# Kernel tuning notes

Measured on AMD Instinct MI355X. Metric: run time of the kernel, lower is better.

The kernel has to match this reference:

```python
import jax, jax.numpy as jnp
import numpy as np


def setup_inputs() -> dict:
    key = jax.random.key(0)
    ks = jax.random.split(key, 7)
    B, T, DIN, D = 64, 512, 512, 512
    s_in = 1.0 / np.sqrt(DIN)  # ~glorot-ish scale for input kernels
    s_h = 1.0 / np.sqrt(D)     # scale for recurrent kernels (orthogonal-ish magnitude)
    return {
        "X": jax.random.normal(ks[0], (B, T, DIN), jnp.float32),
        "W_z": jax.random.normal(ks[1], (DIN, D), jnp.float32) * s_in,
        "U_z": jax.random.normal(ks[2], (D, D), jnp.float32) * s_h,
        "b_z": jnp.zeros((D,), jnp.float32),
        "W_r": jax.random.normal(ks[3], (DIN, D), jnp.float32) * s_in,
        "U_r": jax.random.normal(ks[4], (D, D), jnp.float32) * s_h,
        "b_r": jnp.zeros((D,), jnp.float32),
        "W_h": jax.random.normal(ks[5], (DIN, D), jnp.float32) * s_in,
        "U_h": jax.random.normal(ks[6], (D, D), jnp.float32) * s_h,
        "b_h": jnp.zeros((D,), jnp.float32),
        "mask": jnp.ones((B, T), jnp.int32),
    }


def reference(X, W_z, U_z, b_z, W_r, U_r, b_r, W_h, U_h, b_h, mask):
    # X: [B, T, DIN] -> time-major [T, B, DIN]
    Xt = jnp.transpose(X, (1, 0, 2))
    # Precompute input projections (large GEMMs, done once): [T, B, D]
    xz = Xt @ W_z + b_z
    xr = Xt @ W_r + b_r
    xh = Xt @ W_h + b_h
    # Padded/shifted mask (pad=1): step t sees mask[t-1]; step 0 sees 0,
    # which zeroes the (zero) initial state exactly as in the theano code.
    m = jnp.transpose(mask, (1, 0)).astype(X.dtype)[:, :, None]  # [T, B, 1]
    m_tm1 = jnp.concatenate([jnp.zeros_like(m[:1]), m[:-1]], axis=0)

    B = X.shape[0]
    D = W_z.shape[1]
    h0 = jnp.zeros((B, D), X.dtype)

    def step(h_tm1, inputs):
        xz_t, xr_t, xh_t, mt = inputs
        hm = mt * h_tm1                                  # masked previous state
        z = jax.nn.sigmoid(xz_t + hm @ U_z)              # update gate
        r = jax.nn.sigmoid(xr_t + hm @ U_r)              # reset gate
        hh = jnp.tanh(xh_t + (r * hm) @ U_h)             # candidate
        h_t = z * hm + (1.0 - z) * hh
        return h_t, None

    h_last, _ = jax.lax.scan(step, h0, (xz, xr, xh, m_tm1))
    # return_sequences=False -> last hidden state [B, D]
    return h_last
```

## Files before the change

### kernel.cpp

```cpp
#include <hip/hip_runtime.h>
#include <hip/hip_fp16.h>

#define B_   64
#define T_   512
#define DINc 512
#define D_   512
#define NWG  16
#define JS   32

typedef _Float16 half8 __attribute__((ext_vector_type(8)));
typedef _Float16 half4 __attribute__((ext_vector_type(4)));
typedef float   floatx4 __attribute__((ext_vector_type(4)));
typedef unsigned uintx4 __attribute__((ext_vector_type(4)));

#define WAITV(N) asm volatile("s_waitcnt vmcnt(" #N ")" ::: "memory")
#define SCB()    __builtin_amdgcn_sched_barrier(0)

__global__ __launch_bounds__(256) void k_cvtX(const float* __restrict__ X, _Float16* __restrict__ Xh) {
    int idx = blockIdx.x * 256 + threadIdx.x;
    int m  = idx >> 6;
    int k8 = idx & 63;
    int b = m & 63, t = m >> 6;
    const float* src = X + ((size_t)(b * T_ + t)) * DINc + k8 * 8;
    float4 f0 = *(const float4*)(src);
    float4 f1 = *(const float4*)(src + 4);
    half8 h;
    h[0] = (_Float16)f0.x; h[1] = (_Float16)f0.y; h[2] = (_Float16)f0.z; h[3] = (_Float16)f0.w;
    h[4] = (_Float16)f1.x; h[5] = (_Float16)f1.y; h[6] = (_Float16)f1.z; h[7] = (_Float16)f1.w;
    *(half8*)(Xh + (size_t)m * DINc + k8 * 8) = h;
}

__global__ __launch_bounds__(256) void k_cvtW(const float* __restrict__ M0, const float* __restrict__ M1,
                                              const float* __restrict__ M2, _Float16* __restrict__ Mt) {
    __shared__ float tile[64][65];
    int g = blockIdx.z;
    const float* W = (g == 0) ? M0 : ((g == 1) ? M1 : M2);
    int n0 = blockIdx.x * 64, k0 = blockIdx.y * 64;
    int c = threadIdx.x & 63, r4 = threadIdx.x >> 6;
#pragma unroll
    for (int i = 0; i < 16; ++i) {
        int k = r4 + i * 4;
        tile[k][c] = W[(size_t)(k0 + k) * D_ + n0 + c];
    }
    __syncthreads();
    _Float16* out = Mt + (size_t)g * D_ * DINc;
#pragma unroll
    for (int i = 0; i < 16; ++i) {
        int n = r4 + i * 4;
        out[(size_t)(n0 + n) * DINc + k0 + c] = (_Float16)tile[c][n];
    }
}

__global__ __launch_bounds__(256) void k_cvtM(const int* __restrict__ mask, float* __restrict__ maskT) {
    int idx = blockIdx.x * 256 + threadIdx.x;
    int t = idx >> 6, b = idx & 63;
    maskT[idx] = (float)mask[(size_t)b * T_ + t];
}

__global__ __launch_bounds__(256) void k_gemm(const _Float16* __restrict__ Xh, const _Float16* __restrict__ Wt,
                                              const float* __restrict__ bz, const float* __restrict__ br,
                                              const float* __restrict__ bh, _Float16* __restrict__ xprojT) {
    __shared__ _Float16 As[128 * 32];
    __shared__ _Float16 Bs[128 * 32];
    int g = blockIdx.z;
    const _Float16* Wg = Wt + (size_t)g * 512 * 512;
    const float* bias = (g == 0) ? bz : ((g == 1) ? br : bh);
    _Float16* out = xprojT + (size_t)g * 16777216;
    int mb = blockIdx.x * 128, nb = blockIdx.y * 128;
    int tid = threadIdx.x, l = tid & 63, w = tid >> 6;
    int wr = w >> 1, wc = w & 1;
    int lr = l & 15, lg = l >> 4;

    floatx4 acc[4][4] = {};

    int ga0 = tid, ga1 = tid + 256;
    int ra0 = ga0 >> 2, ca0 = (ga0 & 3) * 8;
    int ra1 = ga1 >> 2, ca1 = (ga1 & 3) * 8;

    uint4 pa0, pa1, pb0, pb1;
    pa0 = *(const uint4*)(Xh + (size_t)(mb + ra0) * 512 + ca0);
    pa1 = *(const uint4*)(Xh + (size_t)(mb + ra1) * 512 + ca1);
    pb0 = *(const uint4*)(Wg + (size_t)(nb + ra0) * 512 + ca0);
    pb1 = *(const uint4*)(Wg + (size_t)(nb + ra1) * 512 + ca1);

    for (int kt = 0; kt < 16; ++kt) {
        __syncthreads();
        *(uint4*)(&As[ga0 * 8]) = pa0;
        *(uint4*)(&As[ga1 * 8]) = pa1;
        *(uint4*)(&Bs[ga0 * 8]) = pb0;
        *(uint4*)(&Bs[ga1 * 8]) = pb1;
        __syncthreads();
        if (kt < 15) {
            int kb = (kt + 1) * 32;
            pa0 = *(const uint4*)(Xh + (size_t)(mb + ra0) * 512 + kb + ca0);
            pa1 = *(const uint4*)(Xh + (size_t)(mb + ra1) * 512 + kb + ca1);
            pb0 = *(const uint4*)(Wg + (size_t)(nb + ra0) * 512 + kb + ca0);
            pb1 = *(const uint4*)(Wg + (size_t)(nb + ra1) * 512 + kb + ca1);
        }
        half8 af[4], bf[4];
#pragma unroll
        for (int mi = 0; mi < 4; mi++) af[mi] = *(const half8*)(&As[(wr * 64 + mi * 16 + lr) * 32 + lg * 8]);
#pragma unroll
        for (int ni = 0; ni < 4; ni++) bf[ni] = *(const half8*)(&Bs[(wc * 64 + ni * 16 + lr) * 32 + lg * 8]);
#pragma unroll
        for (int mi = 0; mi < 4; mi++)
#pragma unroll
            for (int ni = 0; ni < 4; ni++)
                acc[mi][ni] = __builtin_amdgcn_mfma_f32_16x16x32_f16(af[mi], bf[ni], acc[mi][ni], 0, 0, 0);
    }

#pragma unroll
    for (int ni = 0; ni < 4; ni++) {
        int col = nb + wc * 64 + ni * 16 + lr;
        float bv = bias[col];
#pragma unroll
        for (int mi = 0; mi < 4; mi++) {
            int row = mb + wr * 64 + mi * 16 + lg * 4;
            int tt = row >> 6, bb = row & 63;
            half4 hv;
#pragma unroll
            for (int i = 0; i < 4; i++) hv[i] = (_Float16)(acc[mi][ni][i] + bv);
            *(half4*)(out + (size_t)tt * 32768 + (size_t)col * 64 + bb) = hv;
        }
    }
}

__device__ __forceinline__ void st_agent(unsigned long long* p, unsigned long long v) {
    __hip_atomic_store(p, v, __ATOMIC_RELAXED, __HIP_MEMORY_SCOPE_AGENT);
}
__device__ __forceinline__ unsigned ld_flag(const unsigned* p) {
    return __hip_atomic_load(p, __ATOMIC_RELAXED, __HIP_MEMORY_SCOPE_AGENT);
}
__device__ __forceinline__ void st_flag(unsigned* p, unsigned v) {
    __hip_atomic_store(p, v, __ATOMIC_RELAXED, __HIP_MEMORY_SCOPE_AGENT);
}
__device__ __forceinline__ uintx4 ld16_agent(const void* p) {
    uintx4 r;
    asm volatile("global_load_dwordx4 %0, %1, off sc0 sc1" : "=v"(r) : "v"(p) : "memory");
    return r;
}

__device__ __forceinline__ unsigned long long pack_quad(const float v4[4], int lr) {
    unsigned long long unit = 0;
    int j = lr & 3;
#pragma unroll
    for (int i = 0; i < 4; i++) {
        _Float16 hv = (_Float16)v4[i];
        unsigned int v = (unsigned int)__builtin_bit_cast(unsigned short, hv);
        unsigned int o1 = __shfl_xor(v, 1, 64);
        unsigned int pair = (lr & 1) ? (o1 | (v << 16)) : (v | (o1 << 16));
        unsigned int q2 = __shfl_xor(pair, 2, 64);
        unsigned long long u = (lr & 2) ? ((unsigned long long)q2 | ((unsigned long long)pair << 32))
                                        : ((unsigned long long)pair | ((unsigned long long)q2 << 32));
        if (i == j) unit = u;
    }
    return unit;
}

__device__ __forceinline__ void poll_flags(const unsigned* f, unsigned need, int l) {
    for (;;) {
        unsigned v0 = ld_flag(f + l * 16);
        unsigned v1 = ld_flag(f + (64 + l) * 16);
        if (__all(v0 >= need && v1 >= need)) break;
    }
    SCB();
}

__global__ __launch_bounds__(512) void k_scan(const _Float16* __restrict__ Ut,
                                              const float* __restrict__ maskT,
                                              const _Float16* __restrict__ xprojT,
                                              unsigned long long* __restrict__ hbuf,
                                              unsigned long long* __restrict__ rhbuf,
                                              unsigned* __restrict__ fh, unsigned* __restrict__ fr,
                                              float* __restrict__ out) {
    __shared__ __align__(16) _Float16 Ulds[2 * JS * 512];
    __shared__ __align__(16) _Float16 Stg[64 * 512];
    char* StgB = (char*)Stg;
    int tid = threadIdx.x, l = tid & 63, w = tid >> 6;
    int lr = l & 15, lg = l >> 4;
    int mt = w >> 1, nt = w & 1;
    int slot = blockIdx.x;
    int jsb = slot * JS;
    const int fidx = slot * 8 + w;

    for (int c = tid; c < 2 * JS * 64; c += 512) {
        int g  = c >> 11;
        int n  = (c >> 6) & 31;
        int k16 = c & 63;
        uintx4 v = *(const uintx4*)(Ut + (size_t)g * 262144 + (size_t)(jsb + n) * 512 + k16 * 8);
        *(uintx4*)((char*)Ulds + g * 32768 + n * 1024 + ((k16 * 16) ^ ((n & 7) << 4))) = v;
    }
    half8 uhf[16];
    {
        const _Float16* UtH = Ut + (size_t)2 * 262144;
        int ncol = jsb + nt * 16 + lr;
#pragma unroll
        for (int j = 0; j < 16; j++)
            uhf[j] = *(const half8*)(UtH + (size_t)ncol * 512 + j * 32 + lg * 8);
    }
    __syncthreads();

    const char* UB = (const char*)Ulds + (nt * 16 + lr) * 1024;
    const int swz = (lr & 7) << 4;

    int row0 = mt * 16 + lg * 4;
    int colg = jsb + nt * 16 + lr;

    float h4[4]  = {0.f, 0.f, 0.f, 0.f};
    float hm4[4] = {0.f, 0.f, 0.f, 0.f};

    const int punit = (mt * 16 + lg * 4 + (lr & 3)) * 128 + ((jsb + nt * 16) >> 2) + ((lr >> 2) & 3);
    const char* SB = StgB + (mt * 16 + lr) * 1024;

    const _Float16* xzB = xprojT + (size_t)colg * 64 + row0;
    const _Float16* xrB = xzB + (size_t)16777216;
    const _Float16* xhB = xrB + (size_t)16777216;

    {
        half4 xz0 = *(const half4*)(xzB);
        half4 xh0 = *(const half4*)(xhB);
        float4 m0 = *(const float4*)(maskT + row0);
#pragma unroll
        for (int i = 0; i < 4; i++) {
            float z  = __builtin_amdgcn_rcpf(1.f + __expf(-(float)xz0[i]));
            float hh = tanhf((float)xh0[i]);
            h4[i]  = (1.f - z) * hh;
            hm4[i] = ((float)m0[i]) * h4[i];
        }
        st_agent(hbuf + punit, pack_quad(hm4, lr));
        WAITV(0);
        if (l == 0) st_flag(fh + fidx * 16, 1u);
    }

    for (int t = 1; t < T_; ++t) {
        const char* hmG = (const char*)(hbuf + ((t - 1) & 1) * 8192);
        unsigned long long* rhW = rhbuf + (t & 1) * 8192;
        unsigned long long* hW  = hbuf  + (t & 1) * 8192;
        const char* rhG = (const char*)rhW;

        half4 xzp = *(const half4*)(xzB + (size_t)t * 32768);
        half4 xrp = *(const half4*)(xrB + (size_t)t * 32768);
        half4 xhp = *(const half4*)(xhB + (size_t)t * 32768);
        float4 mv = *(const float4*)(maskT + (size_t)t * 64 + row0);

        __syncthreads();
        poll_flags(fh, (unsigned)t, l);
        {
            uintx4 gg[8];
#pragma unroll
            for (int it = 0; it < 8; ++it)
                gg[it] = ld16_agent(hmG + (w * 8 + it) * 1024 + l * 16);
            WAITV(4); SCB();
#pragma unroll
            for (int it = 0; it < 4; ++it)
                *(uintx4*)(StgB + (w * 8 + it) * 1024 + ((l * 16) ^ (it << 4))) = gg[it];
            WAITV(0); SCB();
#pragma unroll
            for (int it = 4; it < 8; ++it)
                *(uintx4*)(StgB + (w * 8 + it) * 1024 + ((l * 16) ^ (it << 4))) = gg[it];
        }
        __syncthreads();
        half8 af[16];
#pragma unroll
        for (int j = 0; j < 16; j++)
            af[j] = *(const half8*)(SB + ((j * 64 + lg * 16) ^ swz));
        floatx4 accr = {0.f, 0.f, 0.f, 0.f};
#pragma unroll
        for (int j = 0; j < 16; j++) {
            int boff = (j * 64 + lg * 16) ^ swz;
            half8 br8 = *(const half8*)(UB + 32768 + boff);
            accr = __builtin_amdgcn_mfma_f32_16x16x32_f16(af[j], br8, accr, 0, 0, 0);
        }
        float rh4[4];
#pragma unroll
        for (int i = 0; i < 4; i++) {
            float rr = __builtin_amdgcn_rcpf(1.f + __expf(-((float)xrp[i] + accr[i])));
            rh4[i] = rr * hm4[i];
        }
        st_agent(rhW + punit, pack_quad(rh4, lr));
        WAITV(0);
        if (l == 0) st_flag(fr + fidx * 16, (unsigned)t);
        floatx4 accz = {0.f, 0.f, 0.f, 0.f};
#pragma unroll
        for (int j = 0; j < 16; j++) {
            int boff = (j * 64 + lg * 16) ^ swz;
            half8 bz8 = *(const half8*)(UB + boff);
            accz = __builtin_amdgcn_mfma_f32_16x16x32_f16(af[j], bz8, accz, 0, 0, 0);
        }
        float z4[4];
#pragma unroll
        for (int i = 0; i < 4; i++)
            z4[i] = __builtin_amdgcn_rcpf(1.f + __expf(-((float)xzp[i] + accz[i])));

        __syncthreads();
        poll_flags(fr, (unsigned)t, l);
        {
            uintx4 gg[8];
#pragma unroll
            for (int it = 0; it < 8; ++it)
                gg[it] = ld16_agent(rhG + (w * 8 + it) * 1024 + l * 16);
            WAITV(4); SCB();
#pragma unroll
            for (int it = 0; it < 4; ++it)
                *(uintx4*)(StgB + (w * 8 + it) * 1024 + ((l * 16) ^ (it << 4))) = gg[it];
            WAITV(0); SCB();
#pragma unroll
            for (int it = 4; it < 8; ++it)
                *(uintx4*)(StgB + (w * 8 + it) * 1024 + ((l * 16) ^ (it << 4))) = gg[it];
        }
        __syncthreads();
        half8 af2[16];
#pragma unroll
        for (int j = 0; j < 16; j++)
            af2[j] = *(const half8*)(SB + ((j * 64 + lg * 16) ^ swz));
        floatx4 acch0 = {0.f, 0.f, 0.f, 0.f}, acch1 = {0.f, 0.f, 0.f, 0.f};
#pragma unroll
        for (int j = 0; j < 16; j += 2) {
            acch0 = __builtin_amdgcn_mfma_f32_16x16x32_f16(af2[j],     uhf[j],     acch0, 0, 0, 0);
            acch1 = __builtin_amdgcn_mfma_f32_16x16x32_f16(af2[j + 1], uhf[j + 1], acch1, 0, 0, 0);
        }
#pragma unroll
        for (int i = 0; i < 4; i++) {
            float hh = tanhf((float)xhp[i] + acch0[i] + acch1[i]);
            h4[i]  = z4[i] * hm4[i] + (1.f - z4[i]) * hh;
            hm4[i] = ((float)mv[i]) * h4[i];
        }
        st_agent(hW + punit, pack_quad(hm4, lr));
        WAITV(0);
        if (l == 0) st_flag(fh + fidx * 16, (unsigned)(t + 1));
    }

#pragma unroll
    for (int i = 0; i < 4; i++)
        out[(size_t)(row0 + i) * 512 + colg] = h4[i];
}

extern "C" void kernel_launch(void* const* d_in, const int* in_sizes, int n_in,
                              void* d_out, int out_size, void* d_ws, size_t ws_size,
                              hipStream_t stream) {
    (void)in_sizes; (void)n_in; (void)out_size; (void)ws_size;
    const float* X  = (const float*)d_in[0];
    const float* Wz = (const float*)d_in[1];
    const float* Uz = (const float*)d_in[2];
    const float* bz = (const float*)d_in[3];
    const float* Wr = (const float*)d_in[4];
    const float* Ur = (const float*)d_in[5];
    const float* br = (const float*)d_in[6];
    const float* Wh = (const float*)d_in[7];
    const float* Uh = (const float*)d_in[8];
    const float* bh = (const float*)d_in[9];
    const int* mask = (const int*)d_in[10];
    float* out = (float*)d_out;

    char* ws = (char*)d_ws;
    unsigned* fh = (unsigned*)ws;
    unsigned* fr = (unsigned*)(ws + 8192);
    unsigned long long* hbuf  = (unsigned long long*)(ws + 16384);
    unsigned long long* rhbuf = (unsigned long long*)(ws + 16384 + 131072);
    _Float16* Xh     = (_Float16*)(ws + 16384 + 2 * 131072);
    _Float16* Wt     = (_Float16*)(ws + 16384 + 2 * 131072 + 33554432);
    _Float16* Ut     = (_Float16*)(ws + 16384 + 2 * 131072 + 33554432 + 1572864);
    _Float16* xprojT = (_Float16*)(ws + 16384 + 2 * 131072 + 33554432 + 2 * 1572864);
    float*    maskT  = (float*)(ws + 16384 + 2 * 131072 + 33554432 + 2 * 1572864 + 100663296);

    hipMemsetAsync(ws, 0, 16384, stream);
    hipLaunchKernelGGL(k_cvtX, dim3(8192), dim3(256), 0, stream, X, Xh);
    hipLaunchKernelGGL(k_cvtW, dim3(8, 8, 3), dim3(256), 0, stream, Wz, Wr, Wh, Wt);
    hipLaunchKernelGGL(k_cvtW, dim3(8, 8, 3), dim3(256), 0, stream, Uz, Ur, Uh, Ut);
    hipLaunchKernelGGL(k_cvtM, dim3(128), dim3(256), 0, stream, mask, maskT);
    hipLaunchKernelGGL(k_gemm, dim3(256, 4, 3), dim3(256), 0, stream, Xh, Wt, bz, br, bh, xprojT);
    hipLaunchKernelGGL(k_scan, dim3(NWG), dim3(512), 0, stream, Ut, maskT, xprojT,
                       hbuf, rhbuf, fh, fr, out);
}
```

Measured before the change: 3.764 ms.

## Halve scan workgroups to 8, each covering 64 hidden columns with 2 row tiles

The persistent recurrent scan now runs on 8 workgroups of 64 hidden columns each instead of 16 of 32. Each wave covers one 16-column tile across two 16-row batch tiles. U_r and U_h live in registers and only U_z stays in LDS. Fewer participants should make the per-step cross-workgroup flag polling cheaper (one flag load per lane instead of two). In exchange, each workgroup does twice the MFMA work per step on the serial critical path and carries more register pressure.

```diff
diff --git a/kernel.cpp b/kernel.cpp
--- a/kernel.cpp
+++ b/kernel.cpp
@@ -5,8 +5,8 @@
 #define T_   512
 #define DINc 512
 #define D_   512
-#define NWG  16
-#define JS   32
+#define NWG  8
+#define JS   64
 
 typedef _Float16 half8 __attribute__((ext_vector_type(8)));
 typedef _Float16 half4 __attribute__((ext_vector_type(4)));
@@ -159,9 +159,8 @@
 
 __device__ __forceinline__ void poll_flags(const unsigned* f, unsigned need, int l) {
     for (;;) {
-        unsigned v0 = ld_flag(f + l * 16);
-        unsigned v1 = ld_flag(f + (64 + l) * 16);
-        if (__all(v0 >= need && v1 >= need)) break;
+        unsigned v = ld_flag(f + l * 16);
+        if (__all(v >= need)) break;
     }
     SCB();
 }
@@ -173,61 +172,71 @@
                                               unsigned long long* __restrict__ rhbuf,
                                               unsigned* __restrict__ fh, unsigned* __restrict__ fr,
                                               float* __restrict__ out) {
-    __shared__ __align__(16) _Float16 Ulds[2 * JS * 512];
+    __shared__ __align__(16) _Float16 Ulds[JS * 512];
     __shared__ __align__(16) _Float16 Stg[64 * 512];
     char* StgB = (char*)Stg;
     int tid = threadIdx.x, l = tid & 63, w = tid >> 6;
     int lr = l & 15, lg = l >> 4;
-    int mt = w >> 1, nt = w & 1;
+    int nt  = w >> 1;
+    int mt2 = w & 1;
+    int m0 = mt2 * 16, m1 = m0 + 32;
     int slot = blockIdx.x;
     int jsb = slot * JS;
     const int fidx = slot * 8 + w;
 
-    for (int c = tid; c < 2 * JS * 64; c += 512) {
-        int g  = c >> 11;
-        int n  = (c >> 6) & 31;
+    for (int c = tid; c < JS * 64; c += 512) {
+        int n   = c >> 6;
         int k16 = c & 63;
-        uintx4 v = *(const uintx4*)(Ut + (size_t)g * 262144 + (size_t)(jsb + n) * 512 + k16 * 8);
-        *(uintx4*)((char*)Ulds + g * 32768 + n * 1024 + ((k16 * 16) ^ ((n & 7) << 4))) = v;
-    }
-    half8 uhf[16];
+        uintx4 v = *(const uintx4*)(Ut + (size_t)(jsb + n) * 512 + k16 * 8);
+        *(uintx4*)((char*)Ulds + n * 1024 + ((k16 * 16) ^ ((n & 7) << 4))) = v;
+    }
+    half8 urf[16], uhf[16];
     {
+        const _Float16* UtR = Ut + (size_t)262144;
         const _Float16* UtH = Ut + (size_t)2 * 262144;
         int ncol = jsb + nt * 16 + lr;
 #pragma unroll
-        for (int j = 0; j < 16; j++)
+        for (int j = 0; j < 16; j++) {
+            urf[j] = *(const half8*)(UtR + (size_t)ncol * 512 + j * 32 + lg * 8);
             uhf[j] = *(const half8*)(UtH + (size_t)ncol * 512 + j * 32 + lg * 8);
+        }
     }
     __syncthreads();
 
     const char* UB = (const char*)Ulds + (nt * 16 + lr) * 1024;
     const int swz = (lr & 7) << 4;
 
-    int row0 = mt * 16 + lg * 4;
     int colg = jsb + nt * 16 + lr;
-
-    float h4[4]  = {0.f, 0.f, 0.f, 0.f};
-    float hm4[4] = {0.f, 0.f, 0.f, 0.f};
-
-    const int punit = (mt * 16 + lg * 4 + (lr & 3)) * 128 + ((jsb + nt * 16) >> 2) + ((lr >> 2) & 3);
-    const char* SB = StgB + (mt * 16 + lr) * 1024;
-
-    const _Float16* xzB = xprojT + (size_t)colg * 64 + row0;
+    int row0 = m0 + lg * 4;
+    int row1 = m1 + lg * 4;
+
+    float h4[2][4]  = {};
+    float hm4[2][4] = {};
+
+    const int punit0 = (m0 + lg * 4 + (lr & 3)) * 128 + ((jsb + nt * 16) >> 2) + ((lr >> 2) & 3);
+    const int punit1 = (m1 + lg * 4 + (lr & 3)) * 128 + ((jsb + nt * 16) >> 2) + ((lr >> 2) & 3);
+    const char* SB0 = StgB + (m0 + lr) * 1024;
+    const char* SB1 = StgB + (m1 + lr) * 1024;
+
+    const _Float16* xzB = xprojT + (size_t)colg * 64;
     const _Float16* xrB = xzB + (size_t)16777216;
     const _Float16* xhB = xrB + (size_t)16777216;
 
     {
-        half4 xz0 = *(const half4*)(xzB);
-        half4 xh0 = *(const half4*)(xhB);
-        float4 m0 = *(const float4*)(maskT + row0);
+        half4 xz0a = *(const half4*)(xzB + row0), xz0b = *(const half4*)(xzB + row1);
+        half4 xh0a = *(const half4*)(xhB + row0), xh0b = *(const half4*)(xhB + row1);
+        float4 m0a = *(const float4*)(maskT + row0), m0b = *(const float4*)(maskT + row1);
 #pragma unroll
         for (int i = 0; i < 4; i++) {
-            float z  = __builtin_amdgcn_rcpf(1.f + __expf(-(float)xz0[i]));
-            float hh = tanhf((float)xh0[i]);
-            h4[i]  = (1.f - z) * hh;
-            hm4[i] = ((float)m0[i]) * h4[i];
-        }
-        st_agent(hbuf + punit, pack_quad(hm4, lr));
+            float za = __builtin_amdgcn_rcpf(1.f + __expf(-(float)xz0a[i]));
+            float zb = __builtin_amdgcn_rcpf(1.f + __expf(-(float)xz0b[i]));
+            h4[0][i] = (1.f - za) * tanhf((float)xh0a[i]);
+            h4[1][i] = (1.f - zb) * tanhf((float)xh0b[i]);
+            hm4[0][i] = ((float)m0a[i]) * h4[0][i];
+            hm4[1][i] = ((float)m0b[i]) * h4[1][i];
+        }
+        st_agent(hbuf + punit0, pack_quad(hm4[0], lr));
+        st_agent(hbuf + punit1, pack_quad(hm4[1], lr));
         WAITV(0);
         if (l == 0) st_flag(fh + fidx * 16, 1u);
     }
@@ -238,10 +247,14 @@
         unsigned long long* hW  = hbuf  + (t & 1) * 8192;
         const char* rhG = (const char*)rhW;
 
-        half4 xzp = *(const half4*)(xzB + (size_t)t * 32768);
-        half4 xrp = *(const half4*)(xrB + (size_t)t * 32768);
-        half4 xhp = *(const half4*)(xhB + (size_t)t * 32768);
-        float4 mv = *(const float4*)(maskT + (size_t)t * 64 + row0);
+        const _Float16* xzT = xzB + (size_t)t * 32768;
+        const _Float16* xrT = xrB + (size_t)t * 32768;
+        const _Float16* xhT = xhB + (size_t)t * 32768;
+        half4 xzp0 = *(const half4*)(xzT + row0), xzp1 = *(const half4*)(xzT + row1);
+        half4 xrp0 = *(const half4*)(xrT + row0), xrp1 = *(const half4*)(xrT + row1);
+        half4 xhp0 = *(const half4*)(xhT + row0), xhp1 = *(const half4*)(xhT + row1);
+        float4 mva = *(const float4*)(maskT + (size_t)t * 64 + row0);
+        float4 mvb = *(const float4*)(maskT + (size_t)t * 64 + row1);
 
         __syncthreads();
         poll_flags(fh, (unsigned)t, l);
@@ -260,37 +273,43 @@
                 *(uintx4*)(StgB + (w * 8 + it) * 1024 + ((l * 16) ^ (it << 4))) = gg[it];
         }
         __syncthreads();
-        half8 af[16];
-#pragma unroll
-        for (int j = 0; j < 16; j++)
-            af[j] = *(const half8*)(SB + ((j * 64 + lg * 16) ^ swz));
-        floatx4 accr = {0.f, 0.f, 0.f, 0.f};
+        floatx4 accr0 = {}, accr1 = {};
+#pragma unroll
+        for (int j = 0; j < 16; j++) {
+            int aoff = (j * 64 + lg * 16) ^ swz;
+            half8 a0 = *(const half8*)(SB0 + aoff);
+            half8 a1 = *(const half8*)(SB1 + aoff);
+            accr0 = __builtin_amdgcn_mfma_f32_16x16x32_f16(a0, urf[j], accr0, 0, 0, 0);
+            accr1 = __builtin_amdgcn_mfma_f32_16x16x32_f16(a1, urf[j], accr1, 0, 0, 0);
+        }
+        float rh4[2][4];
+#pragma unroll
+        for (int i = 0; i < 4; i++) {
+            float r0 = __builtin_amdgcn_rcpf(1.f + __expf(-((float)xrp0[i] + accr0[i])));
+            float r1 = __builtin_amdgcn_rcpf(1.f + __expf(-((float)xrp1[i] + accr1[i])));
+            rh4[0][i] = r0 * hm4[0][i];
+            rh4[1][i] = r1 * hm4[1][i];
+        }
+        st_agent(rhW + punit0, pack_quad(rh4[0], lr));
+        st_agent(rhW + punit1, pack_quad(rh4[1], lr));
+        WAITV(0);
+        if (l == 0) st_flag(fr + fidx * 16, (unsigned)t);
+        floatx4 accz0 = {}, accz1 = {};
 #pragma unroll
         for (int j = 0; j < 16; j++) {
             int boff = (j * 64 + lg * 16) ^ swz;
-            half8 br8 = *(const half8*)(UB + 32768 + boff);
-            accr = __builtin_amdgcn_mfma_f32_16x16x32_f16(af[j], br8, accr, 0, 0, 0);
-        }
-        float rh4[4];
+            half8 a0 = *(const half8*)(SB0 + boff);
+            half8 a1 = *(const half8*)(SB1 + boff);
+            half8 bz = *(const half8*)(UB + boff);
+            accz0 = __builtin_amdgcn_mfma_f32_16x16x32_f16(a0, bz, accz0, 0, 0, 0);
+            accz1 = __builtin_amdgcn_mfma_f32_16x16x32_f16(a1, bz, accz1, 0, 0, 0);
+        }
+        float z4[2][4];
 #pragma unroll
         for (int i = 0; i < 4; i++) {
-            float rr = __builtin_amdgcn_rcpf(1.f + __expf(-((float)xrp[i] + accr[i])));
-            rh4[i] = rr * hm4[i];
-        }
-        st_agent(rhW + punit, pack_quad(rh4, lr));
-        WAITV(0);
-        if (l == 0) st_flag(fr + fidx * 16, (unsigned)t);
-        floatx4 accz = {0.f, 0.f, 0.f, 0.f};
-#pragma unroll
-        for (int j = 0; j < 16; j++) {
-            int boff = (j * 64 + lg * 16) ^ swz;
-            half8 bz8 = *(const half8*)(UB + boff);
-            accz = __builtin_amdgcn_mfma_f32_16x16x32_f16(af[j], bz8, accz, 0, 0, 0);
-        }
-        float z4[4];
-#pragma unroll
-        for (int i = 0; i < 4; i++)
-            z4[i] = __builtin_amdgcn_rcpf(1.f + __expf(-((float)xzp[i] + accz[i])));
+            z4[0][i] = __builtin_amdgcn_rcpf(1.f + __expf(-((float)xzp0[i] + accz0[i])));
+            z4[1][i] = __builtin_amdgcn_rcpf(1.f + __expf(-((float)xzp1[i] + accz1[i])));
+        }
 
         __syncthreads();
         poll_flags(fr, (unsigned)t, l);
@@ -309,30 +328,35 @@
                 *(uintx4*)(StgB + (w * 8 + it) * 1024 + ((l * 16) ^ (it << 4))) = gg[it];
         }
         __syncthreads();
-        half8 af2[16];
-#pragma unroll
-        for (int j = 0; j < 16; j++)
-            af2[j] = *(const half8*)(SB + ((j * 64 + lg * 16) ^ swz));
-        floatx4 acch0 = {0.f, 0.f, 0.f, 0.f}, acch1 = {0.f, 0.f, 0.f, 0.f};
-#pragma unroll
-        for (int j = 0; j < 16; j += 2) {
-            acch0 = __builtin_amdgcn_mfma_f32_16x16x32_f16(af2[j],     uhf[j],     acch0, 0, 0, 0);
-            acch1 = __builtin_amdgcn_mfma_f32_16x16x32_f16(af2[j + 1], uhf[j + 1], acch1, 0, 0, 0);
+        floatx4 acch0 = {}, acch1 = {};
+#pragma unroll
+        for (int j = 0; j < 16; j++) {
+            int aoff = (j * 64 + lg * 16) ^ swz;
+            half8 a0 = *(const half8*)(SB0 + aoff);
+            half8 a1 = *(const half8*)(SB1 + aoff);
+            acch0 = __builtin_amdgcn_mfma_f32_16x16x32_f16(a0, uhf[j], acch0, 0, 0, 0);
+            acch1 = __builtin_amdgcn_mfma_f32_16x16x32_f16(a1, uhf[j], acch1, 0, 0, 0);
         }
 #pragma unroll
         for (int i = 0; i < 4; i++) {
-            float hh = tanhf((float)xhp[i] + acch0[i] + acch1[i]);
-            h4[i]  = z4[i] * hm4[i] + (1.f - z4[i]) * hh;
-            hm4[i] = ((float)mv[i]) * h4[i];
-        }
-        st_agent(hW + punit, pack_quad(hm4, lr));
+            float hha = tanhf((float)xhp0[i] + acch0[i]);
+            float hhb = tanhf((float)xhp1[i] + acch1[i]);
+            h4[0][i] = z4[0][i] * hm4[0][i] + (1.f - z4[0][i]) * hha;
+            h4[1][i] = z4[1][i] * hm4[1][i] + (1.f - z4[1][i]) * hhb;
+            hm4[0][i] = ((float)mva[i]) * h4[0][i];
+            hm4[1][i] = ((float)mvb[i]) * h4[1][i];
+        }
+        st_agent(hW + punit0, pack_quad(hm4[0], lr));
+        st_agent(hW + punit1, pack_quad(hm4[1], lr));
         WAITV(0);
         if (l == 0) st_flag(fh + fidx * 16, (unsigned)(t + 1));
     }
 
 #pragma unroll
-    for (int i = 0; i < 4; i++)
-        out[(size_t)(row0 + i) * 512 + colg] = h4[i];
+    for (int i = 0; i < 4; i++) {
+        out[(size_t)(row0 + i) * 512 + colg] = h4[0][i];
+        out[(size_t)(row1 + i) * 512 + colg] = h4[1][i];
+    }
 }
 
 extern "C" void kernel_launch(void* const* d_in, const int* in_sizes, int n_in,
```

Result: slower. 6.244 ms (+65.9%).

## Compute full reset gate redundantly per workgroup to drop second grid barrier

Applied to the files above, without the earlier changes.

Each workgroup now computes the entire 64x512 reset-gate product r = sigmoid(xr + hm@U_r) locally, streaming U_r from global memory, and forms r*hm in shared memory. This removes the second cross-workgroup exchange (rhbuf store, fr flag and poll) each timestep, halving grid-wide synchronization on the serial critical path. In exchange every workgroup does 16x redundant MFMA work and reads all of U_r (512 KB) from L2 each step, plus many extra xr loads. The final timestep also skips its unnecessary state publish.

```diff
diff --git a/kernel.cpp b/kernel.cpp
--- a/kernel.cpp
+++ b/kernel.cpp
@@ -170,55 +170,61 @@
                                               const float* __restrict__ maskT,
                                               const _Float16* __restrict__ xprojT,
                                               unsigned long long* __restrict__ hbuf,
-                                              unsigned long long* __restrict__ rhbuf,
-                                              unsigned* __restrict__ fh, unsigned* __restrict__ fr,
+                                              unsigned* __restrict__ fh,
                                               float* __restrict__ out) {
-    __shared__ __align__(16) _Float16 Ulds[2 * JS * 512];
+    __shared__ __align__(16) _Float16 UzL[JS * 512];
     __shared__ __align__(16) _Float16 Stg[64 * 512];
     char* StgB = (char*)Stg;
     int tid = threadIdx.x, l = tid & 63, w = tid >> 6;
     int lr = l & 15, lg = l >> 4;
-    int mt = w >> 1, nt = w & 1;
+    int mz = w >> 1, nz = w & 1;
     int slot = blockIdx.x;
     int jsb = slot * JS;
     const int fidx = slot * 8 + w;
 
-    for (int c = tid; c < 2 * JS * 64; c += 512) {
-        int g  = c >> 11;
-        int n  = (c >> 6) & 31;
+    for (int c = tid; c < JS * 64; c += 512) {
+        int n   = c >> 6;
         int k16 = c & 63;
-        uintx4 v = *(const uintx4*)(Ut + (size_t)g * 262144 + (size_t)(jsb + n) * 512 + k16 * 8);
-        *(uintx4*)((char*)Ulds + g * 32768 + n * 1024 + ((k16 * 16) ^ ((n & 7) << 4))) = v;
+        uintx4 v = *(const uintx4*)(Ut + (size_t)(jsb + n) * 512 + k16 * 8);
+        *(uintx4*)((char*)UzL + n * 1024 + ((k16 * 16) ^ ((n & 7) << 4))) = v;
     }
     half8 uhf[16];
     {
         const _Float16* UtH = Ut + (size_t)2 * 262144;
-        int ncol = jsb + nt * 16 + lr;
+        int ncol = jsb + nz * 16 + lr;
 #pragma unroll
         for (int j = 0; j < 16; j++)
             uhf[j] = *(const half8*)(UtH + (size_t)ncol * 512 + j * 32 + lg * 8);
     }
     __syncthreads();
 
-    const char* UB = (const char*)Ulds + (nt * 16 + lr) * 1024;
     const int swz = (lr & 7) << 4;
-
-    int row0 = mt * 16 + lg * 4;
-    int colg = jsb + nt * 16 + lr;
+    const char* SA0 = StgB + (0  + lr) * 1024;
+    const char* SA1 = StgB + (16 + lr) * 1024;
+    const char* SA2 = StgB + (32 + lr) * 1024;
+    const char* SA3 = StgB + (48 + lr) * 1024;
+    const char* SAz = StgB + (mz * 16 + lr) * 1024;
+    const char* UBz = (const char*)UzL + (nz * 16 + lr) * 1024;
+    const _Float16* urB0 = Ut + 262144 + (size_t)(w * 64 +  0 + lr) * 512 + lg * 8;
+    const _Float16* urB1 = Ut + 262144 + (size_t)(w * 64 + 16 + lr) * 512 + lg * 8;
+    const _Float16* urB2 = Ut + 262144 + (size_t)(w * 64 + 32 + lr) * 512 + lg * 8;
+    const _Float16* urB3 = Ut + 262144 + (size_t)(w * 64 + 48 + lr) * 512 + lg * 8;
+
+    int row0 = mz * 16 + lg * 4;
+    int colg = jsb + nz * 16 + lr;
 
     float h4[4]  = {0.f, 0.f, 0.f, 0.f};
     float hm4[4] = {0.f, 0.f, 0.f, 0.f};
 
-    const int punit = (mt * 16 + lg * 4 + (lr & 3)) * 128 + ((jsb + nt * 16) >> 2) + ((lr >> 2) & 3);
-    const char* SB = StgB + (mt * 16 + lr) * 1024;
-
-    const _Float16* xzB = xprojT + (size_t)colg * 64 + row0;
-    const _Float16* xrB = xzB + (size_t)16777216;
-    const _Float16* xhB = xrB + (size_t)16777216;
+    const int punit = (mz * 16 + lg * 4 + (lr & 3)) * 128 + ((jsb + nz * 16) >> 2) + ((lr >> 2) & 3);
+
+    const _Float16* xzB = xprojT + (size_t)colg * 64;
+    const _Float16* xhB = xzB + (size_t)2 * 16777216;
+    const _Float16* xrG = xprojT + (size_t)16777216;
 
     {
-        half4 xz0 = *(const half4*)(xzB);
-        half4 xh0 = *(const half4*)(xhB);
+        half4 xz0 = *(const half4*)(xzB + row0);
+        half4 xh0 = *(const half4*)(xhB + row0);
         float4 m0 = *(const float4*)(maskT + row0);
 #pragma unroll
         for (int i = 0; i < 4; i++) {
@@ -234,13 +240,10 @@
 
     for (int t = 1; t < T_; ++t) {
         const char* hmG = (const char*)(hbuf + ((t - 1) & 1) * 8192);
-        unsigned long long* rhW = rhbuf + (t & 1) * 8192;
-        unsigned long long* hW  = hbuf  + (t & 1) * 8192;
-        const char* rhG = (const char*)rhW;
-
-        half4 xzp = *(const half4*)(xzB + (size_t)t * 32768);
-        half4 xrp = *(const half4*)(xrB + (size_t)t * 32768);
-        half4 xhp = *(const half4*)(xhB + (size_t)t * 32768);
+        unsigned long long* hW = hbuf + (t & 1) * 8192;
+
+        half4 xzp = *(const half4*)(xzB + (size_t)t * 32768 + row0);
+        half4 xhp = *(const half4*)(xhB + (size_t)t * 32768 + row0);
         float4 mv = *(const float4*)(maskT + (size_t)t * 64 + row0);
 
         __syncthreads();
@@ -260,74 +263,98 @@
                 *(uintx4*)(StgB + (w * 8 + it) * 1024 + ((l * 16) ^ (it << 4))) = gg[it];
         }
         __syncthreads();
-        half8 af[16];
-#pragma unroll
-        for (int j = 0; j < 16; j++)
-            af[j] = *(const half8*)(SB + ((j * 64 + lg * 16) ^ swz));
-        floatx4 accr = {0.f, 0.f, 0.f, 0.f};
+
+        floatx4 racc[4][4] = {};
+        floatx4 zacc = {};
+        half8 bb0 = *(const half8*)(urB0);
+        half8 bb1 = *(const half8*)(urB1);
+        half8 bb2 = *(const half8*)(urB2);
+        half8 bb3 = *(const half8*)(urB3);
 #pragma unroll
         for (int j = 0; j < 16; j++) {
-            int boff = (j * 64 + lg * 16) ^ swz;
-            half8 br8 = *(const half8*)(UB + 32768 + boff);
-            accr = __builtin_amdgcn_mfma_f32_16x16x32_f16(af[j], br8, accr, 0, 0, 0);
-        }
-        float rh4[4];
+            int aoff = (j * 64 + lg * 16) ^ swz;
+            half8 a0 = *(const half8*)(SA0 + aoff);
+            half8 a1 = *(const half8*)(SA1 + aoff);
+            half8 a2 = *(const half8*)(SA2 + aoff);
+            half8 a3 = *(const half8*)(SA3 + aoff);
+            half8 az = *(const half8*)(SAz + aoff);
+            half8 bz = *(const half8*)(UBz + aoff);
+            half8 nb0, nb1, nb2, nb3;
+            if (j < 15) {
+                nb0 = *(const half8*)(urB0 + (j + 1) * 32);
+                nb1 = *(const half8*)(urB1 + (j + 1) * 32);
+                nb2 = *(const half8*)(urB2 + (j + 1) * 32);
+                nb3 = *(const half8*)(urB3 + (j + 1) * 32);
+            }
+            zacc = __builtin_amdgcn_mfma_f32_16x16x32_f16(az, bz, zacc, 0, 0, 0);
+            racc[0][0] = __builtin_amdgcn_mfma_f32_16x16x32_f16(a0, bb0, racc[0][0], 0, 0, 0);
+            racc[1][0] = __builtin_amdgcn_mfma_f32_16x16x32_f16(a1, bb0, racc[1][0], 0, 0, 0);
+            racc[2][0] = __builtin_amdgcn_mfma_f32_16x16x32_f16(a2, bb0, racc[2][0], 0, 0, 0);
+            racc[3][0] = __builtin_amdgcn_mfma_f32_16x16x32_f16(a3, bb0, racc[3][0], 0, 0, 0);
+            racc[0][1] = __builtin_amdgcn_mfma_f32_16x16x32_f16(a0, bb1, racc[0][1], 0, 0, 0);
+            racc[1][1] = __builtin_amdgcn_mfma_f32_16x16x32_f16(a1, bb1, racc[1][1], 0, 0, 0);
+            racc[2][1] = __builtin_amdgcn_mfma_f32_16x16x32_f16(a2, bb1, racc[2][1], 0, 0, 0);
+            racc[3][1] = __builtin_amdgcn_mfma_f32_16x16x32_f16(a3, bb1, racc[3][1], 0, 0, 0);
+            racc[0][2] = __builtin_amdgcn_mfma_f32_16x16x32_f16(a0, bb2, racc[0][2], 0, 0, 0);
+            racc[1][2] = __builtin_amdgcn_mfma_f32_16x16x32_f16(a1, bb2, racc[1][2], 0, 0, 0);
+            racc[2][2] = __builtin_amdgcn_mfma_f32_16x16x32_f16(a2, bb2, racc[2][2], 0, 0, 0);
+            racc[3][2] = __builtin_amdgcn_mfma_f32_16x16x32_f16(a3, bb2, racc[3][2], 0, 0, 0);
+            racc[0][3] = __builtin_amdgcn_mfma_f32_16x16x32_f16(a0, bb3, racc[0][3], 0, 0, 0);
+            racc[1][3] = __builtin_amdgcn_mfma_f32_16x16x32_f16(a1, bb3, racc[1][3], 0, 0, 0);
+            racc[2][3] = __builtin_amdgcn_mfma_f32_16x16x32_f16(a2, bb3, racc[2][3], 0, 0, 0);
+            racc[3][3] = __builtin_amdgcn_mfma_f32_16x16x32_f16(a3, bb3, racc[3][3], 0, 0, 0);
+            if (j < 15) { bb0 = nb0; bb1 = nb1; bb2 = nb2; bb3 = nb3; }
+        }
+        float z4[4];
+#pragma unroll
+        for (int i = 0; i < 4; i++)
+            z4[i] = __builtin_amdgcn_rcpf(1.f + __expf(-((float)xzp[i] + zacc[i])));
+
+#pragma unroll
+        for (int m = 0; m < 4; m++)
+#pragma unroll
+            for (int nn = 0; nn < 4; nn++) {
+                half4 xr = *(const half4*)(xrG + (size_t)t * 32768 +
+                                           (size_t)(w * 64 + nn * 16 + lr) * 64 + m * 16 + lg * 4);
+#pragma unroll
+                for (int i = 0; i < 4; i++)
+                    racc[m][nn][i] = __builtin_amdgcn_rcpf(1.f + __expf(-((float)xr[i] + racc[m][nn][i])));
+            }
+        __syncthreads();
+
+#pragma unroll
+        for (int m = 0; m < 4; m++)
+#pragma unroll
+            for (int nn = 0; nn < 4; nn++) {
+                float tmp[4] = {racc[m][nn][0], racc[m][nn][1], racc[m][nn][2], racc[m][nn][3]};
+                unsigned long long u = pack_quad(tmp, lr);
+                int R  = m * 16 + lg * 4 + (lr & 3);
+                int c0 = w * 64 + nn * 16 + ((lr >> 2) & 3) * 4;
+                int byteoff = R * 1024 + (((c0 >> 3) * 16) ^ ((R & 7) << 4)) + ((c0 & 4) ? 8 : 0);
+                half4 hmu = *(half4*)(StgB + byteoff);
+                half4 ru  = __builtin_bit_cast(half4, u);
+                half4 prod = ru * hmu;
+                *(half4*)(StgB + byteoff) = prod;
+            }
+        __syncthreads();
+
+        floatx4 acch = {};
+#pragma unroll
+        for (int j = 0; j < 16; j++) {
+            half8 ah = *(const half8*)(SAz + ((j * 64 + lg * 16) ^ swz));
+            acch = __builtin_amdgcn_mfma_f32_16x16x32_f16(ah, uhf[j], acch, 0, 0, 0);
+        }
 #pragma unroll
         for (int i = 0; i < 4; i++) {
-            float rr = __builtin_amdgcn_rcpf(1.f + __expf(-((float)xrp[i] + accr[i])));
-            rh4[i] = rr * hm4[i];
-        }
-        st_agent(rhW + punit, pack_quad(rh4, lr));
-        WAITV(0);
-        if (l == 0) st_flag(fr + fidx * 16, (unsigned)t);
-        floatx4 accz = {0.f, 0.f, 0.f, 0.f};
-#pragma unroll
-        for (int j = 0; j < 16; j++) {
-            int boff = (j * 64 + lg * 16) ^ swz;
-            half8 bz8 = *(const half8*)(UB + boff);
-            accz = __builtin_amdgcn_mfma_f32_16x16x32_f16(af[j], bz8, accz, 0, 0, 0);
-        }
-        float z4[4];
-#pragma unroll
-        for (int i = 0; i < 4; i++)
-            z4[i] = __builtin_amdgcn_rcpf(1.f + __expf(-((float)xzp[i] + accz[i])));
-
-        __syncthreads();
-        poll_flags(fr, (unsigned)t, l);
-        {
-            uintx4 gg[8];
-#pragma unroll
-            for (int it = 0; it < 8; ++it)
-                gg[it] = ld16_agent(rhG + (w * 8 + it) * 1024 + l * 16);
-            WAITV(4); SCB();
-#pragma unroll
-            for (int it = 0; it < 4; ++it)
-                *(uintx4*)(StgB + (w * 8 + it) * 1024 + ((l * 16) ^ (it << 4))) = gg[it];
-            WAITV(0); SCB();
-#pragma unroll
-            for (int it = 4; it < 8; ++it)
-                *(uintx4*)(StgB + (w * 8 + it) * 1024 + ((l * 16) ^ (it << 4))) = gg[it];
-        }
-        __syncthreads();
-        half8 af2[16];
-#pragma unroll
-        for (int j = 0; j < 16; j++)
-            af2[j] = *(const half8*)(SB + ((j * 64 + lg * 16) ^ swz));
-        floatx4 acch0 = {0.f, 0.f, 0.f, 0.f}, acch1 = {0.f, 0.f, 0.f, 0.f};
-#pragma unroll
-        for (int j = 0; j < 16; j += 2) {
-            acch0 = __builtin_amdgcn_mfma_f32_16x16x32_f16(af2[j],     uhf[j],     acch0, 0, 0, 0);
-            acch1 = __builtin_amdgcn_mfma_f32_16x16x32_f16(af2[j + 1], uhf[j + 1], acch1, 0, 0, 0);
-        }
-#pragma unroll
-        for (int i = 0; i < 4; i++) {
-            float hh = tanhf((float)xhp[i] + acch0[i] + acch1[i]);
+            float hh = tanhf((float)xhp[i] + acch[i]);
             h4[i]  = z4[i] * hm4[i] + (1.f - z4[i]) * hh;
             hm4[i] = ((float)mv[i]) * h4[i];
         }
-        st_agent(hW + punit, pack_quad(hm4, lr));
-        WAITV(0);
-        if (l == 0) st_flag(fh + fidx * 16, (unsigned)(t + 1));
+        if (t < T_ - 1) {
+            st_agent(hW + punit, pack_quad(hm4, lr));
+            WAITV(0);
+            if (l == 0) st_flag(fh + fidx * 16, (unsigned)(t + 1));
+        }
     }
 
 #pragma unroll
@@ -354,9 +381,7 @@
 
     char* ws = (char*)d_ws;
     unsigned* fh = (unsigned*)ws;
-    unsigned* fr = (unsigned*)(ws + 8192);
     unsigned long long* hbuf  = (unsigned long long*)(ws + 16384);
-    unsigned long long* rhbuf = (unsigned long long*)(ws + 16384 + 131072);
     _Float16* Xh     = (_Float16*)(ws + 16384 + 2 * 131072);
     _Float16* Wt     = (_Float16*)(ws + 16384 + 2 * 131072 + 33554432);
     _Float16* Ut     = (_Float16*)(ws + 16384 + 2 * 131072 + 33554432 + 1572864);
@@ -370,5 +395,5 @@
     hipLaunchKernelGGL(k_cvtM, dim3(128), dim3(256), 0, stream, mask, maskT);
     hipLaunchKernelGGL(k_gemm, dim3(256, 4, 3), dim3(256), 0, stream, Xh, Wt, bz, br, bh, xprojT);
     hipLaunchKernelGGL(k_scan, dim3(NWG), dim3(512), 0, stream, Ut, maskT, xprojT,
-                       hbuf, rhbuf, fh, fr, out);
-}
+                       hbuf, fh, out);
+}
```

New measurement: 14.57 ms. +287.1%, slower.

## Replace flag-based cross-workgroup sync with poisoned-data polling in GRU scan

Applied to the files above, without the earlier changes.

Removes the per-wave flag stores and flag polling between workgroups. Consumers now poll the exchanged h and r*h buffers directly until no 16-byte chunk holds the all-ones poison pattern, and each workgroup re-poisons the previous parity buffer after reading it. The aim is to cut one round trip and the waitcnt serialization from every cross-CU handoff in the latency-bound recurrence, and it also raises wave priority around the MFMA loops. The risk is correctness: a valid fp16 pair could be mistaken for poison, and the relaxed re-poison stores could race with peers that have not yet read the buffer.

```diff
diff --git a/kernel.cpp b/kernel.cpp
--- a/kernel.cpp
+++ b/kernel.cpp
@@ -128,16 +128,13 @@
 __device__ __forceinline__ void st_agent(unsigned long long* p, unsigned long long v) {
     __hip_atomic_store(p, v, __ATOMIC_RELAXED, __HIP_MEMORY_SCOPE_AGENT);
 }
-__device__ __forceinline__ unsigned ld_flag(const unsigned* p) {
-    return __hip_atomic_load(p, __ATOMIC_RELAXED, __HIP_MEMORY_SCOPE_AGENT);
-}
-__device__ __forceinline__ void st_flag(unsigned* p, unsigned v) {
-    __hip_atomic_store(p, v, __ATOMIC_RELAXED, __HIP_MEMORY_SCOPE_AGENT);
-}
 __device__ __forceinline__ uintx4 ld16_agent(const void* p) {
     uintx4 r;
     asm volatile("global_load_dwordx4 %0, %1, off sc0 sc1" : "=v"(r) : "v"(p) : "memory");
     return r;
+}
+__device__ __forceinline__ bool chunk_valid(uintx4 v) {
+    return ((v[0] & v[1]) != 0xFFFFFFFFu) && ((v[2] & v[3]) != 0xFFFFFFFFu);
 }
 
 __device__ __forceinline__ unsigned long long pack_quad(const float v4[4], int lr) {
@@ -157,21 +154,11 @@
     return unit;
 }
 
-__device__ __forceinline__ void poll_flags(const unsigned* f, unsigned need, int l) {
-    for (;;) {
-        unsigned v0 = ld_flag(f + l * 16);
-        unsigned v1 = ld_flag(f + (64 + l) * 16);
-        if (__all(v0 >= need && v1 >= need)) break;
-    }
-    SCB();
-}
-
 __global__ __launch_bounds__(512) void k_scan(const _Float16* __restrict__ Ut,
                                               const float* __restrict__ maskT,
                                               const _Float16* __restrict__ xprojT,
                                               unsigned long long* __restrict__ hbuf,
                                               unsigned long long* __restrict__ rhbuf,
-                                              unsigned* __restrict__ fh, unsigned* __restrict__ fr,
                                               float* __restrict__ out) {
     __shared__ __align__(16) _Float16 Ulds[2 * JS * 512];
     __shared__ __align__(16) _Float16 Stg[64 * 512];
@@ -181,7 +168,6 @@
     int mt = w >> 1, nt = w & 1;
     int slot = blockIdx.x;
     int jsb = slot * JS;
-    const int fidx = slot * 8 + w;
 
     for (int c = tid; c < 2 * JS * 64; c += 512) {
         int g  = c >> 11;
@@ -228,14 +214,14 @@
             hm4[i] = ((float)m0[i]) * h4[i];
         }
         st_agent(hbuf + punit, pack_quad(hm4, lr));
-        WAITV(0);
-        if (l == 0) st_flag(fh + fidx * 16, 1u);
     }
 
     for (int t = 1; t < T_; ++t) {
         const char* hmG = (const char*)(hbuf + ((t - 1) & 1) * 8192);
-        unsigned long long* rhW = rhbuf + (t & 1) * 8192;
-        unsigned long long* hW  = hbuf  + (t & 1) * 8192;
+        unsigned long long* rhPsn = rhbuf + ((t - 1) & 1) * 8192;
+        unsigned long long* hPsn  = hbuf  + ((t - 1) & 1) * 8192;
+        unsigned long long* rhW   = rhbuf + (t & 1) * 8192;
+        unsigned long long* hW    = hbuf  + (t & 1) * 8192;
         const char* rhG = (const char*)rhW;
 
         half4 xzp = *(const half4*)(xzB + (size_t)t * 32768);
@@ -243,34 +229,44 @@
         half4 xhp = *(const half4*)(xhB + (size_t)t * 32768);
         float4 mv = *(const float4*)(maskT + (size_t)t * 64 + row0);
 
-        __syncthreads();
-        poll_flags(fh, (unsigned)t, l);
+        uintx4 gg[8];
         {
-            uintx4 gg[8];
+            unsigned vmask = 0;
 #pragma unroll
             for (int it = 0; it < 8; ++it)
                 gg[it] = ld16_agent(hmG + (w * 8 + it) * 1024 + l * 16);
-            WAITV(4); SCB();
-#pragma unroll
-            for (int it = 0; it < 4; ++it)
-                *(uintx4*)(StgB + (w * 8 + it) * 1024 + ((l * 16) ^ (it << 4))) = gg[it];
             WAITV(0); SCB();
 #pragma unroll
-            for (int it = 4; it < 8; ++it)
-                *(uintx4*)(StgB + (w * 8 + it) * 1024 + ((l * 16) ^ (it << 4))) = gg[it];
-        }
+            for (int it = 0; it < 8; ++it) if (chunk_valid(gg[it])) vmask |= 1u << it;
+            while (!__all(vmask == 255u)) {
+#pragma unroll
+                for (int it = 0; it < 8; ++it)
+                    if (!(vmask & (1u << it)))
+                        gg[it] = ld16_agent(hmG + (w * 8 + it) * 1024 + l * 16);
+                WAITV(0); SCB();
+#pragma unroll
+                for (int it = 0; it < 8; ++it) if (chunk_valid(gg[it])) vmask |= 1u << it;
+            }
+        }
+        st_agent(rhPsn + punit, ~0ull);
+        __syncthreads();
+#pragma unroll
+        for (int it = 0; it < 8; ++it)
+            *(uintx4*)(StgB + (w * 8 + it) * 1024 + ((l * 16) ^ (it << 4))) = gg[it];
         __syncthreads();
         half8 af[16];
 #pragma unroll
         for (int j = 0; j < 16; j++)
             af[j] = *(const half8*)(SB + ((j * 64 + lg * 16) ^ swz));
         floatx4 accr = {0.f, 0.f, 0.f, 0.f};
+        __builtin_amdgcn_s_setprio(1);
 #pragma unroll
         for (int j = 0; j < 16; j++) {
             int boff = (j * 64 + lg * 16) ^ swz;
             half8 br8 = *(const half8*)(UB + 32768 + boff);
             accr = __builtin_amdgcn_mfma_f32_16x16x32_f16(af[j], br8, accr, 0, 0, 0);
         }
+        __builtin_amdgcn_s_setprio(0);
         float rh4[4];
 #pragma unroll
         for (int i = 0; i < 4; i++) {
@@ -278,56 +274,65 @@
             rh4[i] = rr * hm4[i];
         }
         st_agent(rhW + punit, pack_quad(rh4, lr));
-        WAITV(0);
-        if (l == 0) st_flag(fr + fidx * 16, (unsigned)t);
         floatx4 accz = {0.f, 0.f, 0.f, 0.f};
+        __builtin_amdgcn_s_setprio(1);
 #pragma unroll
         for (int j = 0; j < 16; j++) {
             int boff = (j * 64 + lg * 16) ^ swz;
             half8 bz8 = *(const half8*)(UB + boff);
             accz = __builtin_amdgcn_mfma_f32_16x16x32_f16(af[j], bz8, accz, 0, 0, 0);
         }
+        __builtin_amdgcn_s_setprio(0);
         float z4[4];
 #pragma unroll
         for (int i = 0; i < 4; i++)
             z4[i] = __builtin_amdgcn_rcpf(1.f + __expf(-((float)xzp[i] + accz[i])));
 
-        __syncthreads();
-        poll_flags(fr, (unsigned)t, l);
+        uintx4 gg2[8];
         {
-            uintx4 gg[8];
+            unsigned vmask = 0;
 #pragma unroll
             for (int it = 0; it < 8; ++it)
-                gg[it] = ld16_agent(rhG + (w * 8 + it) * 1024 + l * 16);
-            WAITV(4); SCB();
-#pragma unroll
-            for (int it = 0; it < 4; ++it)
-                *(uintx4*)(StgB + (w * 8 + it) * 1024 + ((l * 16) ^ (it << 4))) = gg[it];
+                gg2[it] = ld16_agent(rhG + (w * 8 + it) * 1024 + l * 16);
             WAITV(0); SCB();
 #pragma unroll
-            for (int it = 4; it < 8; ++it)
-                *(uintx4*)(StgB + (w * 8 + it) * 1024 + ((l * 16) ^ (it << 4))) = gg[it];
-        }
+            for (int it = 0; it < 8; ++it) if (chunk_valid(gg2[it])) vmask |= 1u << it;
+            while (!__all(vmask == 255u)) {
+#pragma unroll
+                for (int it = 0; it < 8; ++it)
+                    if (!(vmask & (1u << it)))
+                        gg2[it] = ld16_agent(rhG + (w * 8 + it) * 1024 + l * 16);
+                WAITV(0); SCB();
+#pragma unroll
+                for (int it = 0; it < 8; ++it) if (chunk_valid(gg2[it])) vmask |= 1u << it;
+            }
+        }
+        st_agent(hPsn + punit, ~0ull);
+        __syncthreads();
+#pragma unroll
+        for (int it = 0; it < 8; ++it)
+            *(uintx4*)(StgB + (w * 8 + it) * 1024 + ((l * 16) ^ (it << 4))) = gg2[it];
         __syncthreads();
         half8 af2[16];
 #pragma unroll
         for (int j = 0; j < 16; j++)
             af2[j] = *(const half8*)(SB + ((j * 64 + lg * 16) ^ swz));
         floatx4 acch0 = {0.f, 0.f, 0.f, 0.f}, acch1 = {0.f, 0.f, 0.f, 0.f};
+        __builtin_amdgcn_s_setprio(1);
 #pragma unroll
         for (int j = 0; j < 16; j += 2) {
             acch0 = __builtin_amdgcn_mfma_f32_16x16x32_f16(af2[j],     uhf[j],     acch0, 0, 0, 0);
             acch1 = __builtin_amdgcn_mfma_f32_16x16x32_f16(af2[j + 1], uhf[j + 1], acch1, 0, 0, 0);
         }
+        __builtin_amdgcn_s_setprio(0);
 #pragma unroll
         for (int i = 0; i < 4; i++) {
             float hh = tanhf((float)xhp[i] + acch0[i] + acch1[i]);
             h4[i]  = z4[i] * hm4[i] + (1.f - z4[i]) * hh;
             hm4[i] = ((float)mv[i]) * h4[i];
         }
-        st_agent(hW + punit, pack_quad(hm4, lr));
-        WAITV(0);
-        if (l == 0) st_flag(fh + fidx * 16, (unsigned)(t + 1));
+        if (t < T_ - 1)
+            st_agent(hW + punit, pack_quad(hm4, lr));
     }
 
 #pragma unroll
@@ -353,8 +358,6 @@
     float* out = (float*)d_out;
 
     char* ws = (char*)d_ws;
-    unsigned* fh = (unsigned*)ws;
-    unsigned* fr = (unsigned*)(ws + 8192);
     unsigned long long* hbuf  = (unsigned long long*)(ws + 16384);
     unsigned long long* rhbuf = (unsigned long long*)(ws + 16384 + 131072);
     _Float16* Xh     = (_Float16*)(ws + 16384 + 2 * 131072);
@@ -363,12 +366,12 @@
     _Float16* xprojT = (_Float16*)(ws + 16384 + 2 * 131072 + 33554432 + 2 * 1572864);
     float*    maskT  = (float*)(ws + 16384 + 2 * 131072 + 33554432 + 2 * 1572864 + 100663296);
 
-    hipMemsetAsync(ws, 0, 16384, stream);
+    hipMemsetAsync(ws + 16384, 0xFF, 2 * 131072, stream);
     hipLaunchKernelGGL(k_cvtX, dim3(8192), dim3(256), 0, stream, X, Xh);
     hipLaunchKernelGGL(k_cvtW, dim3(8, 8, 3), dim3(256), 0, stream, Wz, Wr, Wh, Wt);
     hipLaunchKernelGGL(k_cvtW, dim3(8, 8, 3), dim3(256), 0, stream, Uz, Ur, Uh, Ut);
     hipLaunchKernelGGL(k_cvtM, dim3(128), dim3(256), 0, stream, mask, maskT);
     hipLaunchKernelGGL(k_gemm, dim3(256, 4, 3), dim3(256), 0, stream, Xh, Wt, bz, br, bh, xprojT);
     hipLaunchKernelGGL(k_scan, dim3(NWG), dim3(512), 0, stream, Ut, maskT, xprojT,
-                       hbuf, rhbuf, fh, fr, out);
-}
+                       hbuf, rhbuf, out);
+}
```

New measurement: 4.256 ms. 1.13x slower.
